# Kernel optimization log

Hardware: AMD Instinct MI355X
Metric: run time of the kernel (lower is better)

## Reference

```python
import jax, jax.numpy as jnp
import numpy as np

EMBED_SIZE = 1024
HEADS = 16
HEAD_DIM = EMBED_SIZE // HEADS  # 64


def setup_inputs() -> dict:
    key = jax.random.key(0)
    k_x, k_q, k_k, k_v, k_o, k_b = jax.random.split(key, 6)
    B, S = 32, 8192  # S divisible by HEADS
    x = jax.random.normal(k_x, (B, S, HEAD_DIM), dtype=jnp.float32)
    # torch.nn.Linear weights are [out, in]; scale ~ 1/sqrt(fan_in)
    s_h = 1.0 / np.sqrt(HEAD_DIM)
    s_e = 1.0 / np.sqrt(EMBED_SIZE)
    Wq = jax.random.uniform(k_q, (HEAD_DIM, HEAD_DIM), jnp.float32, -s_h, s_h)
    Wk = jax.random.uniform(k_k, (HEAD_DIM, HEAD_DIM), jnp.float32, -s_h, s_h)
    Wv = jax.random.uniform(k_v, (HEAD_DIM, HEAD_DIM), jnp.float32, -s_h, s_h)
    Wo = jax.random.uniform(k_o, (EMBED_SIZE, EMBED_SIZE), jnp.float32, -s_e, s_e)
    bo = jax.random.uniform(k_b, (EMBED_SIZE,), jnp.float32, -s_e, s_e)
    return {"x": x, "Wq": Wq, "Wk": Wk, "Wv": Wv, "Wo": Wo, "bo": bo}


def reference(x, Wq, Wk, Wv, Wo, bo):
    B = x.shape[0]
    # Q/K/V projections: Linear(head_dim, head_dim), bias=False -> x @ W.T
    Q = (x @ Wq.T).reshape(B, -1, HEADS, HEAD_DIM)  # [B, G, H, D], G = S/H
    K = (x @ Wk.T).reshape(B, -1, HEADS, HEAD_DIM)
    V = (x @ Wv.T).reshape(B, -1, HEADS, HEAD_DIM)
    # energy = Q @ K^T over last two dims -> [B, G, H, H]
    energy = jnp.einsum('bghd,bgkd->bghk', Q, K)
    attn = jax.nn.softmax(energy / jnp.sqrt(jnp.float32(EMBED_SIZE)), axis=3)
    out = jnp.einsum('bghk,bgkd->bghd', attn, V)      # [B, G, H, D]
    out = out.transpose(0, 2, 1, 3).reshape(B, -1, EMBED_SIZE)  # [B, S/H, E]
    return out @ Wo.T + bo
```

## Files before the change

kernel.cpp:

```cpp
#include <hip/hip_runtime.h>
#include <hip/hip_bf16.h>
#include <stdint.h>

#define TOKS   262144
#define NGRP   16384
#define EMB    1024
#define HD     64

using bf16x8 = __attribute__((ext_vector_type(8))) short;
using f32x4  = __attribute__((ext_vector_type(4))) float;

__device__ __forceinline__ unsigned pack2(float a, float b) {
    union { __hip_bfloat162 h; unsigned u; } cvt;
    cvt.h = __float22bfloat162_rn(make_float2(a, b));
    return cvt.u;
}
__device__ __forceinline__ bf16x8 cvt8(float4 v0, float4 v1) {
    uint4 u;
    u.x = pack2(v0.x, v0.y);
    u.y = pack2(v0.z, v0.w);
    u.z = pack2(v1.x, v1.y);
    u.w = pack2(v1.z, v1.w);
    return __builtin_bit_cast(bf16x8, u);
}
__device__ __forceinline__ void gload_lds16(const unsigned short* g, unsigned short* l) {
    __builtin_amdgcn_global_load_lds(
        (const __attribute__((address_space(1))) void*)g,
        (__attribute__((address_space(3))) void*)l,
        16, 0, 0);
}

__global__ __launch_bounds__(256) void k_cvt(const float* __restrict__ wo,
                                             const float* __restrict__ wq,
                                             const float* __restrict__ wk,
                                             const float* __restrict__ wv,
                                             unsigned short* __restrict__ wob,
                                             unsigned short* __restrict__ wqkvb) {
    int bid = blockIdx.x;
    if (bid < 512) {
        int tid = bid * 256 + threadIdx.x;
        int c   = tid >> 12;
        int nb  = (tid >> 6) & 63;
        int l   = tid & 63;
        int n   = nb * 16 + (l & 15);
        int k   = c * 32 + (l >> 4) * 8;
        const float* src = wo + (size_t)n * 1024 + k;
        float4 v0 = *(const float4*)(src);
        float4 v1 = *(const float4*)(src + 4);
        *(bf16x8*)(wob + (size_t)tid * 8) = cvt8(v0, v1);
    } else {
        int b = bid - 512;
        int m = b >> 2;
        const float* src = (m == 0) ? wq : ((m == 1) ? wk : wv);
        int idx = ((b & 3) * 256 + threadIdx.x) * 4;
        float4 v = *(const float4*)(src + idx);
        uint2 p;
        p.x = pack2(v.x, v.y);
        p.y = pack2(v.z, v.w);
        *(uint2*)(wqkvb + m * 4096 + idx) = p;
    }
}

#define SCL 0.0450842200278f

__global__ __launch_bounds__(256) void k_fused(const float* __restrict__ x,
                                               const unsigned short* __restrict__ wqkv,
                                               unsigned short* __restrict__ out2) {
    __shared__ __align__(16) unsigned short qkls[4][2][16 * 72];
    int t = threadIdx.x;
    int w = t >> 6, l = t & 63;
    int c = l & 15, q = l >> 4;
    int waveTok0 = blockIdx.x * 128 + w * 32;

    #pragma unroll 1
    for (int g = 0; g < 2; ++g) {
        bf16x8 xa[2];
        {
            const float* xp = x + (size_t)(waveTok0 + g * 16 + c) * 64 + q * 8;
            #pragma unroll
            for (int kc = 0; kc < 2; ++kc) {
                float4 v0 = *(const float4*)(xp + kc * 32);
                float4 v1 = *(const float4*)(xp + kc * 32 + 4);
                xa[kc] = cvt8(v0, v1);
            }
        }

        uint2 pkV[4];
        #pragma unroll
        for (int m = 0; m < 3; ++m) {
            #pragma unroll
            for (int nb = 0; nb < 4; ++nb) {
                const unsigned short* wp = wqkv + m * 4096 + (nb * 16 + c) * 64 + q * 8;
                bf16x8 w0 = *(const bf16x8*)(wp);
                bf16x8 w1 = *(const bf16x8*)(wp + 32);
                f32x4 acc = (f32x4){0.f, 0.f, 0.f, 0.f};
                acc = __builtin_amdgcn_mfma_f32_16x16x32_bf16(xa[0], w0, acc, 0, 0, 0);
                acc = __builtin_amdgcn_mfma_f32_16x16x32_bf16(xa[1], w1, acc, 0, 0, 0);
                unsigned u01 = pack2(acc[0], acc[1]);
                unsigned u23 = pack2(acc[2], acc[3]);
                if (m < 2) {
                    unsigned short* tile = qkls[w][m];
                    int base = 4 * q * 72 + nb * 16 + c;
                    tile[base]       = (unsigned short)u01;
                    tile[base + 72]  = (unsigned short)(u01 >> 16);
                    tile[base + 144] = (unsigned short)u23;
                    tile[base + 216] = (unsigned short)(u23 >> 16);
                } else {
                    pkV[nb].x = u01;
                    pkV[nb].y = u23;
                }
            }
        }

        f32x4 e = (f32x4){0.f, 0.f, 0.f, 0.f};
        {
            const unsigned short* Qt = qkls[w][0];
            const unsigned short* Kt = qkls[w][1];
            #pragma unroll
            for (int kc = 0; kc < 2; ++kc) {
                bf16x8 ka = *(const bf16x8*)(Kt + c * 72 + kc * 32 + q * 8);
                bf16x8 qb = *(const bf16x8*)(Qt + c * 72 + kc * 32 + q * 8);
                e = __builtin_amdgcn_mfma_f32_16x16x32_bf16(ka, qb, e, 0, 0, 0);
            }
        }

        unsigned pa0, pa1;
        {
            float mx = fmaxf(fmaxf(e[0], e[1]), fmaxf(e[2], e[3]));
            mx = fmaxf(mx, __shfl_xor(mx, 16));
            mx = fmaxf(mx, __shfl_xor(mx, 32));
            float p0 = exp2f((e[0] - mx) * SCL);
            float p1 = exp2f((e[1] - mx) * SCL);
            float p2 = exp2f((e[2] - mx) * SCL);
            float p3 = exp2f((e[3] - mx) * SCL);
            float s = p0 + p1 + p2 + p3;
            s += __shfl_xor(s, 16);
            s += __shfl_xor(s, 32);
            float rinv = 1.0f / s;
            pa0 = pack2(p0 * rinv, p1 * rinv);
            pa1 = pack2(p2 * rinv, p3 * rinv);
        }

        int s0 = (32 * q + c) & 63;
        int s1 = (32 * q + 16 + c) & 63;
        int v0 = 32 * (q & 1) + c;
        int v1 = v0 + 16;
        bool hi = (q >= 2);
        {
            int a0 = __shfl((int)pa0, s0);
            int a1 = __shfl((int)pa1, s0);
            int a2 = __shfl((int)pa0, s1);
            int a3 = __shfl((int)pa1, s1);
            uint4 A2u;
            A2u.x = hi ? 0u : (unsigned)a0;
            A2u.y = hi ? 0u : (unsigned)a1;
            A2u.z = hi ? 0u : (unsigned)a2;
            A2u.w = hi ? 0u : (unsigned)a3;
            bf16x8 A2 = __builtin_bit_cast(bf16x8, A2u);

            unsigned short* Ot = qkls[w][0];
            #pragma unroll
            for (int nb = 0; nb < 4; ++nb) {
                uint4 B2u;
                B2u.x = (unsigned)__shfl((int)pkV[nb].x, v0);
                B2u.y = (unsigned)__shfl((int)pkV[nb].y, v0);
                B2u.z = (unsigned)__shfl((int)pkV[nb].x, v1);
                B2u.w = (unsigned)__shfl((int)pkV[nb].y, v1);
                bf16x8 B2 = __builtin_bit_cast(bf16x8, B2u);
                f32x4 o = (f32x4){0.f, 0.f, 0.f, 0.f};
                o = __builtin_amdgcn_mfma_f32_16x16x32_bf16(A2, B2, o, 0, 0, 0);
                unsigned u01 = pack2(o[0], o[1]);
                unsigned u23 = pack2(o[2], o[3]);
                int base = 4 * q * 72 + nb * 16 + c;
                Ot[base]       = (unsigned short)u01;
                Ot[base + 72]  = (unsigned short)(u01 >> 16);
                Ot[base + 144] = (unsigned short)u23;
                Ot[base + 216] = (unsigned short)(u23 >> 16);
            }
        }

        {
            int gi = (waveTok0 >> 4) + g;
            int b    = gi >> 9;
            int grem = gi & 511;
            int rowbase = b * 512 + (grem >> 4);
            int colpref = (grem & 15) * 64;
            const unsigned short* osrc = qkls[w][0] + (l >> 2) * 72 + (l & 3) * 16;
            uint4 ov0 = *(const uint4*)(osrc);
            uint4 ov1 = *(const uint4*)(osrc + 8);
            unsigned short* dst = out2 + (size_t)(rowbase + (l >> 2) * 32) * 1024
                                       + colpref + (l & 3) * 16;
            *(uint4*)(dst)     = ov0;
            *(uint4*)(dst + 8) = ov1;
        }
    }
}

#define STG(gb, lb, half, kt) do { \
    gload_lds16((gb) + (size_t)(half) * 131072 + (size_t)(kt) * 64 + ga0, \
                (lb) + (half) * 8192 + lo0); \
    gload_lds16((gb) + (size_t)(half) * 131072 + (size_t)(kt) * 64 + ga1, \
                (lb) + (half) * 8192 + lo1); \
} while (0)

#define LDA4(buf, mh) do { \
    _Pragma("unroll") \
    for (int i2 = 0; i2 < 4; ++i2) { \
        const unsigned short* _p = (buf) + (wrow + ((mh) * 4 + i2) * 16 + lm) * 64; \
        a[i2][0] = *(const bf16x8*)(_p + jo0); \
        a[i2][1] = *(const bf16x8*)(_p + jo1); \
    } \
} while (0)

#define GLBB(d, gp) do { \
    _Pragma("unroll") \
    for (int n = 0; n < 4; ++n) { \
        d[n][0] = *(const bf16x8*)((gp) + n * 512); \
        d[n][1] = *(const bf16x8*)((gp) + 32768 + n * 512); \
    } \
} while (0)

#define MM16(mh, B) do { \
    _Pragma("unroll") \
    for (int i2 = 0; i2 < 4; ++i2) { \
        _Pragma("unroll") \
        for (int n = 0; n < 4; ++n) { \
            acc[(mh)*4+i2][n] = __builtin_amdgcn_mfma_f32_16x16x32_bf16( \
                a[i2][0], B[n][0], acc[(mh)*4+i2][n], 0, 0, 0); \
            acc[(mh)*4+i2][n] = __builtin_amdgcn_mfma_f32_16x16x32_bf16( \
                a[i2][1], B[n][1], acc[(mh)*4+i2][n], 0, 0, 0); \
        } \
    } \
} while (0)

#define TILE(_t, cB, nB) do { \
    if ((_t) < 15) GLBB(nB, gB); \
    if ((_t) < 14) { STG(Ab, pAs, 0, (_t) + 2); STG(Ab, pAs, 1, (_t) + 2); } \
    LDA4(pAr, 0); \
    asm volatile("s_waitcnt lgkmcnt(0)" ::: "memory"); \
    __builtin_amdgcn_sched_barrier(0); \
    __builtin_amdgcn_s_setprio(1); \
    MM16(0, cB); \
    __builtin_amdgcn_s_setprio(0); \
    LDA4(pAr, 1); \
    asm volatile("s_waitcnt lgkmcnt(0)" ::: "memory"); \
    __builtin_amdgcn_sched_barrier(0); \
    __builtin_amdgcn_s_setprio(1); \
    MM16(1, cB); \
    __builtin_amdgcn_s_setprio(0); \
    if ((_t) < 14)       { asm volatile("s_waitcnt vmcnt(4)" ::: "memory"); } \
    else if ((_t) == 14) { asm volatile("s_waitcnt vmcnt(0)" ::: "memory"); } \
    __builtin_amdgcn_s_barrier(); \
    { unsigned short* _tmp = pAr; pAr = pAn; pAn = pAs; pAs = _tmp; } \
    gB += 65536; \
} while (0)

__global__ __launch_bounds__(512, 2) void k_gemm256(const unsigned short* __restrict__ A,
                                                    const unsigned short* __restrict__ Bp,
                                                    const float* __restrict__ bias,
                                                    float* __restrict__ C) {
    extern __shared__ __align__(16) unsigned short lds[];
    unsigned short* As0 = lds;
    unsigned short* As1 = lds + 16384;
    unsigned short* As2 = lds + 32768;

    const int t = threadIdx.x;
    const int w = t >> 6, l = t & 63;
    const int lm = l & 15, q4 = l >> 4;
    const int jxor = lm & 7;
    const int jo0 = ((0 + q4) ^ jxor) * 8;
    const int jo1 = ((4 + q4) ^ jxor) * 8;

    const int bid = blockIdx.x;
    const int wg  = (bid & 7) * 32 + (bid >> 3);
    const int m0  = (wg >> 2) * 256;
    const int n0  = (wg & 3) * 256;

    const int wrow = (w >> 2) * 128;
    const int wcol = (w & 3) * 64;

    const int s1 = w * 128 + l;
    const int s2 = s1 + 64;
    const int r0 = s1 >> 3, c0 = s1 & 7;
    const int r1 = s2 >> 3, c1 = s2 & 7;
    const size_t ga0 = (size_t)r0 * 1024 + (size_t)((c0 ^ (r0 & 7)) * 8);
    const size_t ga1 = (size_t)r1 * 1024 + (size_t)((c1 ^ (r1 & 7)) * 8);
    const int lo0 = s1 * 8;
    const int lo1 = s2 * 8;

    const unsigned short* Ab = A + (size_t)m0 * 1024;
    const unsigned short* gB = Bp + (size_t)((n0 >> 4) + (wcol >> 4)) * 512
                                  + (size_t)l * 8;

    f32x4 acc[8][4];
    #pragma unroll
    for (int mi = 0; mi < 8; ++mi)
        #pragma unroll
        for (int ni = 0; ni < 4; ++ni)
            acc[mi][ni] = (f32x4){0.f, 0.f, 0.f, 0.f};

    unsigned short* pAr = As0;
    unsigned short* pAn = As1;
    unsigned short* pAs = As2;

    bf16x8 a[4][2];
    bf16x8 bC[4][2], bN[4][2];

    GLBB(bC, gB);
    STG(Ab, pAr, 0, 0); STG(Ab, pAr, 1, 0);
    STG(Ab, pAn, 0, 1); STG(Ab, pAn, 1, 1);
    asm volatile("s_waitcnt vmcnt(4)" ::: "memory");
    __builtin_amdgcn_s_barrier();
    gB += 65536;

    #pragma unroll 1
    for (int tt = 0; tt < 8; ++tt) {
        TILE(2 * tt,     bC, bN);
        TILE(2 * tt + 1, bN, bC);
    }

    float bc[4];
    #pragma unroll
    for (int ni = 0; ni < 4; ++ni) bc[ni] = bias[n0 + wcol + ni * 16 + lm];
    #pragma unroll
    for (int mi = 0; mi < 8; ++mi) {
        #pragma unroll
        for (int r = 0; r < 4; ++r) {
            const int row = m0 + wrow + mi * 16 + q4 * 4 + r;
            float* cp = C + (size_t)row * 1024 + n0 + wcol + lm;
            #pragma unroll
            for (int ni = 0; ni < 4; ++ni)
                cp[ni * 16] = acc[mi][ni][r] + bc[ni];
        }
    }
}

extern "C" void kernel_launch(void* const* d_in, const int* in_sizes, int n_in,
                              void* d_out, int out_size, void* d_ws, size_t ws_size,
                              hipStream_t stream) {
    const float* x  = (const float*)d_in[0];
    const float* wq = (const float*)d_in[1];
    const float* wk = (const float*)d_in[2];
    const float* wv = (const float*)d_in[3];
    const float* wo = (const float*)d_in[4];
    const float* bo = (const float*)d_in[5];
    float* out = (float*)d_out;

    unsigned short* out2  = (unsigned short*)d_ws;
    unsigned short* wob   = out2 + (size_t)NGRP * 1024;
    unsigned short* wqkvb = wob + (size_t)EMB * EMB;

    static int s_once = []() {
        hipFuncSetAttribute((const void*)k_gemm256,
                            hipFuncAttributeMaxDynamicSharedMemorySize, 98304);
        return 0;
    }();
    (void)s_once;

    k_cvt    <<<524,  256, 0, stream>>>(wo, wq, wk, wv, wob, wqkvb);
    k_fused  <<<2048, 256, 0, stream>>>(x, wqkvb, out2);
    k_gemm256<<<256, 512, 98304, stream>>>(out2, wob, bo, out);
}
```

Baseline: 186.1 us.

## Fuse attention and output projection into single kernel with LDS-resident intermediate

Merges the per-group attention kernel and the output GEMM into one kernel where each block computes a 64-row tile of the attention output, keeps it in LDS with XOR swizzling, then multiplies it by the bf16 Wo streamed directly from global memory. This removes the round trip of the bf16 intermediate through HBM and one kernel launch. In exchange, each block re-reads the full Wo matrix, GEMM tiles are smaller, LDS use forces one block per CU, and B loads are not staged through shared memory.

```diff
diff --git a/kernel.cpp b/kernel.cpp
--- a/kernel.cpp
+++ b/kernel.cpp
@@ -22,12 +22,6 @@
     u.z = pack2(v1.x, v1.y);
     u.w = pack2(v1.z, v1.w);
     return __builtin_bit_cast(bf16x8, u);
-}
-__device__ __forceinline__ void gload_lds16(const unsigned short* g, unsigned short* l) {
-    __builtin_amdgcn_global_load_lds(
-        (const __attribute__((address_space(1))) void*)g,
-        (__attribute__((address_space(3))) void*)l,
-        16, 0, 0);
 }
 
 __global__ __launch_bounds__(256) void k_cvt(const float* __restrict__ wo,
@@ -39,11 +33,11 @@
     int bid = blockIdx.x;
     if (bid < 512) {
         int tid = bid * 256 + threadIdx.x;
-        int c   = tid >> 12;
+        int kc  = tid >> 12;
         int nb  = (tid >> 6) & 63;
         int l   = tid & 63;
         int n   = nb * 16 + (l & 15);
-        int k   = c * 32 + (l >> 4) * 8;
+        int k   = kc * 32 + (l >> 4) * 8;
         const float* src = wo + (size_t)n * 1024 + k;
         float4 v0 = *(const float4*)(src);
         float4 v1 = *(const float4*)(src + 4);
@@ -63,20 +57,34 @@
 
 #define SCL 0.0450842200278f
 
-__global__ __launch_bounds__(256) void k_fused(const float* __restrict__ x,
-                                               const unsigned short* __restrict__ wqkv,
-                                               unsigned short* __restrict__ out2) {
-    __shared__ __align__(16) unsigned short qkls[4][2][16 * 72];
-    int t = threadIdx.x;
-    int w = t >> 6, l = t & 63;
-    int c = l & 15, q = l >> 4;
-    int waveTok0 = blockIdx.x * 128 + w * 32;
+#define MFMA_B16(A, B, Cc) __builtin_amdgcn_mfma_f32_16x16x32_bf16(A, B, Cc, 0, 0, 0)
+
+__global__ __launch_bounds__(512, 2) void k_mega(const float* __restrict__ x,
+                                                 const unsigned short* __restrict__ wqkv,
+                                                 const unsigned short* __restrict__ wob,
+                                                 const float* __restrict__ bias,
+                                                 float* __restrict__ C) {
+    extern __shared__ __align__(16) unsigned short lds[];
+    unsigned short* out2s = lds;
+    unsigned short* kscr  = lds + 65536;
+
+    const int t = threadIdx.x;
+    const int w = t >> 6, l = t & 63;
+    const int c = l & 15, q = l >> 4;
+    const int bid   = blockIdx.x;
+    const int batch = bid >> 3, q8 = bid & 7;
+    unsigned short* kw = kscr + w * 1024;
 
     #pragma unroll 1
-    for (int g = 0; g < 2; ++g) {
+    for (int i = 0; i < 8; ++i) {
+        const int gl   = w * 8 + i;
+        const int gbq  = gl >> 4;
+        const int gcol = gl & 15;
+        const size_t tok0 = (size_t)bid * 1024 + (size_t)gl * 16;
+
         bf16x8 xa[2];
         {
-            const float* xp = x + (size_t)(waveTok0 + g * 16 + c) * 64 + q * 8;
+            const float* xp = x + (tok0 + c) * 64 + q * 8;
             #pragma unroll
             for (int kc = 0; kc < 2; ++kc) {
                 float4 v0 = *(const float4*)(xp + kc * 32);
@@ -84,6 +92,10 @@
                 xa[kc] = cvt8(v0, v1);
             }
         }
+
+        const int mQ0 = gbq << 3;
+        const int mQ1 = 32 + (gbq << 3);
+        unsigned short* qslot = out2s + (size_t)(16 * q + gbq) * 1024 + gcol * 64;
 
         uint2 pkV[4];
         #pragma unroll
@@ -94,17 +106,22 @@
                 bf16x8 w0 = *(const bf16x8*)(wp);
                 bf16x8 w1 = *(const bf16x8*)(wp + 32);
                 f32x4 acc = (f32x4){0.f, 0.f, 0.f, 0.f};
-                acc = __builtin_amdgcn_mfma_f32_16x16x32_bf16(xa[0], w0, acc, 0, 0, 0);
-                acc = __builtin_amdgcn_mfma_f32_16x16x32_bf16(xa[1], w1, acc, 0, 0, 0);
+                acc = MFMA_B16(xa[0], w0, acc);
+                acc = MFMA_B16(xa[1], w1, acc);
                 unsigned u01 = pack2(acc[0], acc[1]);
                 unsigned u23 = pack2(acc[2], acc[3]);
-                if (m < 2) {
-                    unsigned short* tile = qkls[w][m];
-                    int base = 4 * q * 72 + nb * 16 + c;
-                    tile[base]       = (unsigned short)u01;
-                    tile[base + 72]  = (unsigned short)(u01 >> 16);
-                    tile[base + 144] = (unsigned short)u23;
-                    tile[base + 216] = (unsigned short)(u23 >> 16);
+                const int d = nb * 16 + c;
+                if (m == 0) {
+                    qslot[(d ^ mQ0)]              = (unsigned short)u01;
+                    qslot[4 * 1024 + (d ^ mQ1)]   = (unsigned short)(u01 >> 16);
+                    qslot[8 * 1024 + (d ^ mQ0)]   = (unsigned short)u23;
+                    qslot[12 * 1024 + (d ^ mQ1)]  = (unsigned short)(u23 >> 16);
+                } else if (m == 1) {
+                    const int kr = 4 * q;
+                    kw[(kr + 0) * 64 + (d ^ (((kr + 0) & 7) << 3))] = (unsigned short)u01;
+                    kw[(kr + 1) * 64 + (d ^ (((kr + 1) & 7) << 3))] = (unsigned short)(u01 >> 16);
+                    kw[(kr + 2) * 64 + (d ^ (((kr + 2) & 7) << 3))] = (unsigned short)u23;
+                    kw[(kr + 3) * 64 + (d ^ (((kr + 3) & 7) << 3))] = (unsigned short)(u23 >> 16);
                 } else {
                     pkV[nb].x = u01;
                     pkV[nb].y = u23;
@@ -114,13 +131,14 @@
 
         f32x4 e = (f32x4){0.f, 0.f, 0.f, 0.f};
         {
-            const unsigned short* Qt = qkls[w][0];
-            const unsigned short* Kt = qkls[w][1];
+            const int mq = ((c * 4 + gbq) & 7) << 3;
+            const unsigned short* qrow = out2s + (size_t)(c * 4 + gbq) * 1024 + gcol * 64;
             #pragma unroll
             for (int kc = 0; kc < 2; ++kc) {
-                bf16x8 ka = *(const bf16x8*)(Kt + c * 72 + kc * 32 + q * 8);
-                bf16x8 qb = *(const bf16x8*)(Qt + c * 72 + kc * 32 + q * 8);
-                e = __builtin_amdgcn_mfma_f32_16x16x32_bf16(ka, qb, e, 0, 0, 0);
+                const int L = kc * 32 + q * 8;
+                bf16x8 ka = *(const bf16x8*)(kw + c * 64 + (L ^ ((c & 7) << 3)));
+                bf16x8 qb = *(const bf16x8*)(qrow + (L ^ mq));
+                e = MFMA_B16(ka, qb, e);
             }
         }
 
@@ -141,16 +159,16 @@
             pa1 = pack2(p2 * rinv, p3 * rinv);
         }
 
-        int s0 = (32 * q + c) & 63;
-        int s1 = (32 * q + 16 + c) & 63;
-        int v0 = 32 * (q & 1) + c;
-        int v1 = v0 + 16;
-        bool hi = (q >= 2);
-        {
-            int a0 = __shfl((int)pa0, s0);
-            int a1 = __shfl((int)pa1, s0);
-            int a2 = __shfl((int)pa0, s1);
-            int a3 = __shfl((int)pa1, s1);
+        {
+            const int sh0 = (32 * q + c) & 63;
+            const int sh1 = (32 * q + 16 + c) & 63;
+            const int sv0 = 32 * (q & 1) + c;
+            const int sv1 = sv0 + 16;
+            const bool hi = (q >= 2);
+            int a0 = __shfl((int)pa0, sh0);
+            int a1 = __shfl((int)pa1, sh0);
+            int a2 = __shfl((int)pa0, sh1);
+            int a3 = __shfl((int)pa1, sh1);
             uint4 A2u;
             A2u.x = hi ? 0u : (unsigned)a0;
             A2u.y = hi ? 0u : (unsigned)a1;
@@ -158,179 +176,91 @@
             A2u.w = hi ? 0u : (unsigned)a3;
             bf16x8 A2 = __builtin_bit_cast(bf16x8, A2u);
 
-            unsigned short* Ot = qkls[w][0];
             #pragma unroll
             for (int nb = 0; nb < 4; ++nb) {
                 uint4 B2u;
-                B2u.x = (unsigned)__shfl((int)pkV[nb].x, v0);
-                B2u.y = (unsigned)__shfl((int)pkV[nb].y, v0);
-                B2u.z = (unsigned)__shfl((int)pkV[nb].x, v1);
-                B2u.w = (unsigned)__shfl((int)pkV[nb].y, v1);
+                B2u.x = (unsigned)__shfl((int)pkV[nb].x, sv0);
+                B2u.y = (unsigned)__shfl((int)pkV[nb].y, sv0);
+                B2u.z = (unsigned)__shfl((int)pkV[nb].x, sv1);
+                B2u.w = (unsigned)__shfl((int)pkV[nb].y, sv1);
                 bf16x8 B2 = __builtin_bit_cast(bf16x8, B2u);
                 f32x4 o = (f32x4){0.f, 0.f, 0.f, 0.f};
-                o = __builtin_amdgcn_mfma_f32_16x16x32_bf16(A2, B2, o, 0, 0, 0);
+                o = MFMA_B16(A2, B2, o);
                 unsigned u01 = pack2(o[0], o[1]);
                 unsigned u23 = pack2(o[2], o[3]);
-                int base = 4 * q * 72 + nb * 16 + c;
-                Ot[base]       = (unsigned short)u01;
-                Ot[base + 72]  = (unsigned short)(u01 >> 16);
-                Ot[base + 144] = (unsigned short)u23;
-                Ot[base + 216] = (unsigned short)(u23 >> 16);
-            }
-        }
-
-        {
-            int gi = (waveTok0 >> 4) + g;
-            int b    = gi >> 9;
-            int grem = gi & 511;
-            int rowbase = b * 512 + (grem >> 4);
-            int colpref = (grem & 15) * 64;
-            const unsigned short* osrc = qkls[w][0] + (l >> 2) * 72 + (l & 3) * 16;
-            uint4 ov0 = *(const uint4*)(osrc);
-            uint4 ov1 = *(const uint4*)(osrc + 8);
-            unsigned short* dst = out2 + (size_t)(rowbase + (l >> 2) * 32) * 1024
-                                       + colpref + (l & 3) * 16;
-            *(uint4*)(dst)     = ov0;
-            *(uint4*)(dst + 8) = ov1;
-        }
-    }
-}
-
-#define STG(gb, lb, half, kt) do { \
-    gload_lds16((gb) + (size_t)(half) * 131072 + (size_t)(kt) * 64 + ga0, \
-                (lb) + (half) * 8192 + lo0); \
-    gload_lds16((gb) + (size_t)(half) * 131072 + (size_t)(kt) * 64 + ga1, \
-                (lb) + (half) * 8192 + lo1); \
-} while (0)
-
-#define LDA4(buf, mh) do { \
-    _Pragma("unroll") \
-    for (int i2 = 0; i2 < 4; ++i2) { \
-        const unsigned short* _p = (buf) + (wrow + ((mh) * 4 + i2) * 16 + lm) * 64; \
-        a[i2][0] = *(const bf16x8*)(_p + jo0); \
-        a[i2][1] = *(const bf16x8*)(_p + jo1); \
-    } \
-} while (0)
-
-#define GLBB(d, gp) do { \
-    _Pragma("unroll") \
-    for (int n = 0; n < 4; ++n) { \
-        d[n][0] = *(const bf16x8*)((gp) + n * 512); \
-        d[n][1] = *(const bf16x8*)((gp) + 32768 + n * 512); \
-    } \
-} while (0)
-
-#define MM16(mh, B) do { \
-    _Pragma("unroll") \
-    for (int i2 = 0; i2 < 4; ++i2) { \
-        _Pragma("unroll") \
-        for (int n = 0; n < 4; ++n) { \
-            acc[(mh)*4+i2][n] = __builtin_amdgcn_mfma_f32_16x16x32_bf16( \
-                a[i2][0], B[n][0], acc[(mh)*4+i2][n], 0, 0, 0); \
-            acc[(mh)*4+i2][n] = __builtin_amdgcn_mfma_f32_16x16x32_bf16( \
-                a[i2][1], B[n][1], acc[(mh)*4+i2][n], 0, 0, 0); \
-        } \
-    } \
-} while (0)
-
-#define TILE(_t, cB, nB) do { \
-    if ((_t) < 15) GLBB(nB, gB); \
-    if ((_t) < 14) { STG(Ab, pAs, 0, (_t) + 2); STG(Ab, pAs, 1, (_t) + 2); } \
-    LDA4(pAr, 0); \
-    asm volatile("s_waitcnt lgkmcnt(0)" ::: "memory"); \
-    __builtin_amdgcn_sched_barrier(0); \
-    __builtin_amdgcn_s_setprio(1); \
-    MM16(0, cB); \
-    __builtin_amdgcn_s_setprio(0); \
-    LDA4(pAr, 1); \
-    asm volatile("s_waitcnt lgkmcnt(0)" ::: "memory"); \
-    __builtin_amdgcn_sched_barrier(0); \
-    __builtin_amdgcn_s_setprio(1); \
-    MM16(1, cB); \
-    __builtin_amdgcn_s_setprio(0); \
-    if ((_t) < 14)       { asm volatile("s_waitcnt vmcnt(4)" ::: "memory"); } \
-    else if ((_t) == 14) { asm volatile("s_waitcnt vmcnt(0)" ::: "memory"); } \
-    __builtin_amdgcn_s_barrier(); \
-    { unsigned short* _tmp = pAr; pAr = pAn; pAn = pAs; pAs = _tmp; } \
-    gB += 65536; \
-} while (0)
-
-__global__ __launch_bounds__(512, 2) void k_gemm256(const unsigned short* __restrict__ A,
-                                                    const unsigned short* __restrict__ Bp,
-                                                    const float* __restrict__ bias,
-                                                    float* __restrict__ C) {
-    extern __shared__ __align__(16) unsigned short lds[];
-    unsigned short* As0 = lds;
-    unsigned short* As1 = lds + 16384;
-    unsigned short* As2 = lds + 32768;
-
-    const int t = threadIdx.x;
-    const int w = t >> 6, l = t & 63;
-    const int lm = l & 15, q4 = l >> 4;
-    const int jxor = lm & 7;
-    const int jo0 = ((0 + q4) ^ jxor) * 8;
-    const int jo1 = ((4 + q4) ^ jxor) * 8;
-
-    const int bid = blockIdx.x;
-    const int wg  = (bid & 7) * 32 + (bid >> 3);
-    const int m0  = (wg >> 2) * 256;
-    const int n0  = (wg & 3) * 256;
-
-    const int wrow = (w >> 2) * 128;
-    const int wcol = (w & 3) * 64;
-
-    const int s1 = w * 128 + l;
-    const int s2 = s1 + 64;
-    const int r0 = s1 >> 3, c0 = s1 & 7;
-    const int r1 = s2 >> 3, c1 = s2 & 7;
-    const size_t ga0 = (size_t)r0 * 1024 + (size_t)((c0 ^ (r0 & 7)) * 8);
-    const size_t ga1 = (size_t)r1 * 1024 + (size_t)((c1 ^ (r1 & 7)) * 8);
-    const int lo0 = s1 * 8;
-    const int lo1 = s2 * 8;
-
-    const unsigned short* Ab = A + (size_t)m0 * 1024;
-    const unsigned short* gB = Bp + (size_t)((n0 >> 4) + (wcol >> 4)) * 512
-                                  + (size_t)l * 8;
-
-    f32x4 acc[8][4];
-    #pragma unroll
-    for (int mi = 0; mi < 8; ++mi)
-        #pragma unroll
-        for (int ni = 0; ni < 4; ++ni)
-            acc[mi][ni] = (f32x4){0.f, 0.f, 0.f, 0.f};
-
-    unsigned short* pAr = As0;
-    unsigned short* pAn = As1;
-    unsigned short* pAs = As2;
-
-    bf16x8 a[4][2];
-    bf16x8 bC[4][2], bN[4][2];
-
-    GLBB(bC, gB);
-    STG(Ab, pAr, 0, 0); STG(Ab, pAr, 1, 0);
-    STG(Ab, pAn, 0, 1); STG(Ab, pAn, 1, 1);
-    asm volatile("s_waitcnt vmcnt(4)" ::: "memory");
-    __builtin_amdgcn_s_barrier();
-    gB += 65536;
+                const int d = nb * 16 + c;
+                qslot[(d ^ mQ0)]              = (unsigned short)u01;
+                qslot[4 * 1024 + (d ^ mQ1)]   = (unsigned short)(u01 >> 16);
+                qslot[8 * 1024 + (d ^ mQ0)]   = (unsigned short)u23;
+                qslot[12 * 1024 + (d ^ mQ1)]  = (unsigned short)(u23 >> 16);
+            }
+        }
+    }
+
+    __syncthreads();
+
+    const unsigned short* gBw = wob + (size_t)(w * 8) * 512 + (size_t)l * 8;
+    float bc[8];
+    #pragma unroll
+    for (int nb = 0; nb < 8; ++nb) bc[nb] = bias[w * 128 + nb * 16 + c];
+
+    f32x4 acc[4][8];
+    #pragma unroll
+    for (int m = 0; m < 4; ++m)
+        #pragma unroll
+        for (int nb = 0; nb < 8; ++nb)
+            acc[m][nb] = (f32x4){0.f, 0.f, 0.f, 0.f};
+
+    const int axor = (c & 7) << 3;
+    bf16x8 bE[8], bO[8], a[4];
+
+    #pragma unroll
+    for (int nb = 0; nb < 8; ++nb) bE[nb] = *(const bf16x8*)(gBw + nb * 512);
 
     #pragma unroll 1
-    for (int tt = 0; tt < 8; ++tt) {
-        TILE(2 * tt,     bC, bN);
-        TILE(2 * tt + 1, bN, bC);
-    }
-
-    float bc[4];
-    #pragma unroll
-    for (int ni = 0; ni < 4; ++ni) bc[ni] = bias[n0 + wcol + ni * 16 + lm];
-    #pragma unroll
-    for (int mi = 0; mi < 8; ++mi) {
+    for (int tt = 0; tt < 16; ++tt) {
+        const size_t kb = (size_t)tt * 65536;
+        #pragma unroll
+        for (int nb = 0; nb < 8; ++nb)
+            bO[nb] = *(const bf16x8*)(gBw + kb + 32768 + nb * 512);
+        {
+            const int L = (2 * tt) * 32 + q * 8;
+            #pragma unroll
+            for (int m = 0; m < 4; ++m)
+                a[m] = *(const bf16x8*)(out2s + (size_t)(m * 16 + c) * 1024 + (L ^ axor));
+            #pragma unroll
+            for (int m = 0; m < 4; ++m)
+                #pragma unroll
+                for (int nb = 0; nb < 8; ++nb)
+                    acc[m][nb] = MFMA_B16(a[m], bE[nb], acc[m][nb]);
+        }
+        if (tt < 15) {
+            #pragma unroll
+            for (int nb = 0; nb < 8; ++nb)
+                bE[nb] = *(const bf16x8*)(gBw + kb + 65536 + nb * 512);
+        }
+        {
+            const int L = (2 * tt + 1) * 32 + q * 8;
+            #pragma unroll
+            for (int m = 0; m < 4; ++m)
+                a[m] = *(const bf16x8*)(out2s + (size_t)(m * 16 + c) * 1024 + (L ^ axor));
+            #pragma unroll
+            for (int m = 0; m < 4; ++m)
+                #pragma unroll
+                for (int nb = 0; nb < 8; ++nb)
+                    acc[m][nb] = MFMA_B16(a[m], bO[nb], acc[m][nb]);
+        }
+    }
+
+    #pragma unroll
+    for (int m = 0; m < 4; ++m) {
         #pragma unroll
         for (int r = 0; r < 4; ++r) {
-            const int row = m0 + wrow + mi * 16 + q4 * 4 + r;
-            float* cp = C + (size_t)row * 1024 + n0 + wcol + lm;
-            #pragma unroll
-            for (int ni = 0; ni < 4; ++ni)
-                cp[ni * 16] = acc[mi][ni][r] + bc[ni];
+            const int rg = batch * 512 + (m * 4 + q) * 32 + q8 * 4 + r;
+            float* cp = C + (size_t)rg * 1024 + w * 128 + c;
+            #pragma unroll
+            for (int nb = 0; nb < 8; ++nb)
+                cp[nb * 16] = acc[m][nb][r] + bc[nb];
         }
     }
 }
@@ -346,18 +276,16 @@
     const float* bo = (const float*)d_in[5];
     float* out = (float*)d_out;
 
-    unsigned short* out2  = (unsigned short*)d_ws;
-    unsigned short* wob   = out2 + (size_t)NGRP * 1024;
+    unsigned short* wob   = (unsigned short*)d_ws;
     unsigned short* wqkvb = wob + (size_t)EMB * EMB;
 
     static int s_once = []() {
-        hipFuncSetAttribute((const void*)k_gemm256,
-                            hipFuncAttributeMaxDynamicSharedMemorySize, 98304);
+        hipFuncSetAttribute((const void*)k_mega,
+                            hipFuncAttributeMaxDynamicSharedMemorySize, 147456);
         return 0;
     }();
     (void)s_once;
 
-    k_cvt    <<<524,  256, 0, stream>>>(wo, wq, wk, wv, wob, wqkvb);
-    k_fused  <<<2048, 256, 0, stream>>>(x, wqkvb, out2);
-    k_gemm256<<<256, 512, 98304, stream>>>(out2, wob, bo, out);
-}
+    k_cvt <<<524, 256, 0, stream>>>(wo, wq, wk, wv, wob, wqkvb);
+    k_mega<<<256, 512, 147456, stream>>>(x, wqkvb, wob, bo, out);
+}
```

Result: faster. 151.4 us, median of 2 (-18.6%).
